# Performance work log

Measured on AMD Instinct MI355X. Metric: run time of the kernel, lower is better.

The kernel has to match this reference:

```python
import jax, jax.numpy as jnp
import numpy as np

N, IN_DIM, HIDDEN, CLASSES, HEADS, E = 4096, 256, 512, 256, 4, 131072
HD = IN_DIM // HEADS


def setup_inputs() -> dict:
    key = jax.random.key(0)
    ks = jax.random.split(key, 16)
    s = 0.02
    x = jax.random.normal(ks[0], (N, IN_DIM), dtype=jnp.float32)
    edge_index = jax.random.randint(ks[1], (2, E), 0, N, dtype=jnp.int64)
    return {
        "x": x,
        "edge_index": edge_index,
        # GCNConv 1: in_dim -> hidden
        "gcn1_w": jax.random.normal(ks[2], (IN_DIM, HIDDEN), dtype=jnp.float32) * s,
        "gcn1_b": jnp.zeros((HIDDEN,), dtype=jnp.float32),
        # GCNConv 2: hidden -> hidden
        "gcn2_w": jax.random.normal(ks[3], (HIDDEN, HIDDEN), dtype=jnp.float32) * s,
        "gcn2_b": jnp.zeros((HIDDEN,), dtype=jnp.float32),
        # final Linear hidden -> classes
        "lin_w": jax.random.normal(ks[4], (HIDDEN, CLASSES), dtype=jnp.float32) * s,
        "lin_b": jnp.zeros((CLASSES,), dtype=jnp.float32),
        # MultiheadAttention packed in-projection (q,k,v) and out-projection
        "in_proj_w": jax.random.normal(ks[5], (3 * IN_DIM, IN_DIM), dtype=jnp.float32) * s,
        "in_proj_b": jnp.zeros((3 * IN_DIM,), dtype=jnp.float32),
        "out_proj_w": jax.random.normal(ks[6], (IN_DIM, IN_DIM), dtype=jnp.float32) * s,
        "out_proj_b": jnp.zeros((IN_DIM,), dtype=jnp.float32),
        # project: in_dim -> classes
        "proj_w": jax.random.normal(ks[7], (IN_DIM, CLASSES), dtype=jnp.float32) * s,
        "proj_b": jnp.zeros((CLASSES,), dtype=jnp.float32),
    }


def gcn_conv(x, src, dst, norm, w, b):
    # PyG GCNConv: transform, then normalized scatter-add aggregation
    h = x @ w                                   # [N+?, F] -> use gathered below
    msg = h[src] * norm[:, None]                # [E+N, F]
    out = jax.ops.segment_sum(msg, dst, num_segments=N)
    return out + b


def mha(x, in_proj_w, in_proj_b, out_proj_w, out_proj_b):
    qkv = x @ in_proj_w.T + in_proj_b           # [N, 3*IN_DIM]
    q, k, v = jnp.split(qkv, 3, axis=-1)
    # [N, IN_DIM] -> [HEADS, N, HD]
    q = q.reshape(N, HEADS, HD).transpose(1, 0, 2)
    k = k.reshape(N, HEADS, HD).transpose(1, 0, 2)
    v = v.reshape(N, HEADS, HD).transpose(1, 0, 2)
    scores = jnp.einsum("hqd,hkd->hqk", q, k) / jnp.sqrt(jnp.float32(HD))
    attn = jax.nn.softmax(scores, axis=-1)      # [HEADS, N, N]
    o = jnp.einsum("hqk,hkd->hqd", attn, v)     # [HEADS, N, HD]
    o = o.transpose(1, 0, 2).reshape(N, IN_DIM)
    return o @ out_proj_w.T + out_proj_b


def reference(x, edge_index, gcn1_w, gcn1_b, gcn2_w, gcn2_b, lin_w, lin_b,
              in_proj_w, in_proj_b, out_proj_w, out_proj_b, proj_w, proj_b):
    # --- GCN normalization with self-loops (computed once, shared by both convs) ---
    loop = jnp.arange(N, dtype=edge_index.dtype)
    src = jnp.concatenate([edge_index[0], loop])  # [E+N]
    dst = jnp.concatenate([edge_index[1], loop])
    deg = jax.ops.segment_sum(jnp.ones_like(dst, dtype=jnp.float32), dst, num_segments=N)
    dinv = jnp.where(deg > 0, jax.lax.rsqrt(deg), 0.0)
    norm = dinv[src] * dinv[dst]                  # [E+N]

    # --- GNN branch ---
    h = jax.nn.relu(gcn_conv(x, src, dst, norm, gcn1_w, gcn1_b))
    h = jax.nn.relu(gcn_conv(h, src, dst, norm, gcn2_w, gcn2_b))
    x_gnn = h @ lin_w + lin_b                     # [N, CLASSES]

    # --- Transformer branch ---
    x_tf = mha(x, in_proj_w, in_proj_b, out_proj_w, out_proj_b)
    x_proj = x_tf @ proj_w + proj_b               # [N, CLASSES]

    return jax.nn.relu(x_gnn + x_proj)
```

## Files before the change

### kernel.cpp

```cpp
#include <hip/hip_runtime.h>
#include <hip/hip_bf16.h>

#define N_NODES 4096
#define IN_DIM  256
#define HIDDEN  512
#define CLASSES 256
#define HEADS   4
#define HD      64
#define NEDGE   131072
#define NMASK   (N_NODES - 1)

typedef __attribute__((ext_vector_type(8))) short bf16x8_t;
typedef __attribute__((ext_vector_type(4))) float f32x4_t;

__device__ inline ushort f2bf(float f) {
    union { float f; uint u; } v; v.f = f;
    uint r = v.u + 0x7FFF + ((v.u >> 16) & 1);
    return (ushort)(r >> 16);
}
__device__ inline float bf2f(ushort u) {
    union { uint u; float f; } v; v.u = (uint)u << 16; return v.f;
}

__global__ void zero_i_k(int* __restrict__ p, int n) {
    int i = blockIdx.x * 256 + threadIdx.x;
    if (i < n) p[i] = 0;
}
__global__ void hist_k(const int* __restrict__ dst, int* __restrict__ cnt) {
    int i = blockIdx.x * 256 + threadIdx.x;
    if (i < NEDGE) atomicAdd(&cnt[dst[i] & NMASK], 1);
}
__global__ __launch_bounds__(256) void scan_k(const int* __restrict__ cnt,
                                              int* __restrict__ rowptr,
                                              float* __restrict__ dinv) {
    __shared__ int part[256];
    const int t = threadIdx.x;
    const int base = t * 16;
    int local[16];
    int s = 0;
    #pragma unroll
    for (int u = 0; u < 16; ++u) { local[u] = cnt[base + u]; s += local[u]; }
    part[t] = s;
    __syncthreads();
    if (t == 0) {
        int acc = 0;
        for (int i = 0; i < 256; ++i) { int v = part[i]; part[i] = acc; acc += v; }
    }
    __syncthreads();
    int acc = part[t];
    #pragma unroll
    for (int u = 0; u < 16; ++u) {
        rowptr[base + u] = acc;
        acc += local[u];
        dinv[base + u] = rsqrtf((float)local[u] + 1.0f);
    }
    if (t == 255) rowptr[N_NODES] = acc;
}
__global__ void scatter_k(const int* __restrict__ src, const int* __restrict__ dst,
                          const int* __restrict__ rowptr, int* __restrict__ tail,
                          int* __restrict__ ssrc) {
    int e = blockIdx.x * 256 + threadIdx.x;
    if (e >= NEDGE) return;
    int d = dst[e] & NMASK;
    int pos = rowptr[d] + atomicAdd(&tail[d], 1);
    ssrc[pos] = src[e] & NMASK;
}

__global__ void split_k(const float* __restrict__ in, ushort* __restrict__ hi,
                        ushort* __restrict__ lo, int n4) {
    int i = blockIdx.x * 256 + threadIdx.x;
    if (i >= n4) return;
    float4 v = ((const float4*)in)[i];
    ushort4 h, l;
    h.x = f2bf(v.x); l.x = f2bf(v.x - bf2f(h.x));
    h.y = f2bf(v.y); l.y = f2bf(v.y - bf2f(h.y));
    h.z = f2bf(v.z); l.z = f2bf(v.z - bf2f(h.z));
    h.w = f2bf(v.w); l.w = f2bf(v.w - bf2f(h.w));
    ((ushort4*)hi)[i] = h;
    ((ushort4*)lo)[i] = l;
}

__global__ __launch_bounds__(256) void tsplit_k(const float* __restrict__ W,
                                                ushort* __restrict__ th,
                                                ushort* __restrict__ tl,
                                                int K, int N) {
    __shared__ float T[64][68];
    const int k0 = blockIdx.x * 64, n0 = blockIdx.y * 64;
    const int t = threadIdx.x;
    {
        const int r = t >> 2, q = (t & 3) * 16;
        const float* src = W + (size_t)(k0 + r) * N + n0 + q;
        #pragma unroll
        for (int i = 0; i < 4; ++i)
            *(float4*)&T[r][q + i * 4] = *(const float4*)(src + i * 4);
    }
    __syncthreads();
    const int n = t >> 2, kq = (t & 3) * 16;
    ushort hh[16], ll[16];
    #pragma unroll
    for (int i = 0; i < 16; ++i) {
        float v = T[kq + i][n];
        ushort h = f2bf(v);
        hh[i] = h; ll[i] = f2bf(v - bf2f(h));
    }
    ushort* ph = th + (size_t)(n0 + n) * K + k0 + kq;
    ushort* pl = tl + (size_t)(n0 + n) * K + k0 + kq;
    #pragma unroll
    for (int i = 0; i < 16; ++i) { ph[i] = hh[i]; pl[i] = ll[i]; }
}

template<int MODE>
__global__ __launch_bounds__(256) void gemm_sp_k(
    const ushort* __restrict__ Ah, const ushort* __restrict__ Al,
    const ushort* __restrict__ Bh, const ushort* __restrict__ Bl,
    const float* __restrict__ bias, const float* src,
    void* o1, void* o2, void* o3, int M, int N, int K)
{
    __shared__ ushort AsH[64][32], AsL[64][32], BsH[64][32], BsL[64][32];
    const int tid = threadIdx.x;
    const int w = tid >> 6, lane = tid & 63, g = lane >> 4, c = lane & 15;
    const int wr = w >> 1, wc = w & 1;
    const int m0 = blockIdx.x * 64, n0 = blockIdx.y * 64;
    const int sr = tid >> 2, sq = (tid & 3) * 8;

    f32x4_t acc[2][2];
    #pragma unroll
    for (int i = 0; i < 2; ++i)
        #pragma unroll
        for (int j = 0; j < 2; ++j) { acc[i][j][0]=0.f; acc[i][j][1]=0.f; acc[i][j][2]=0.f; acc[i][j][3]=0.f; }

    for (int k0 = 0; k0 < K; k0 += 32) {
        __syncthreads();
        *(bf16x8_t*)&AsH[sr][sq] = *(const bf16x8_t*)(Ah + (size_t)(m0 + sr) * K + k0 + sq);
        *(bf16x8_t*)&AsL[sr][sq] = *(const bf16x8_t*)(Al + (size_t)(m0 + sr) * K + k0 + sq);
        *(bf16x8_t*)&BsH[sr][sq] = *(const bf16x8_t*)(Bh + (size_t)(n0 + sr) * K + k0 + sq);
        *(bf16x8_t*)&BsL[sr][sq] = *(const bf16x8_t*)(Bl + (size_t)(n0 + sr) * K + k0 + sq);
        __syncthreads();

        bf16x8_t aH[2], aL[2], bH[2], bL[2];
        #pragma unroll
        for (int mr = 0; mr < 2; ++mr) {
            aH[mr] = *(const bf16x8_t*)&AsH[wr * 32 + mr * 16 + c][g * 8];
            aL[mr] = *(const bf16x8_t*)&AsL[wr * 32 + mr * 16 + c][g * 8];
        }
        #pragma unroll
        for (int nr = 0; nr < 2; ++nr) {
            bH[nr] = *(const bf16x8_t*)&BsH[wc * 32 + nr * 16 + c][g * 8];
            bL[nr] = *(const bf16x8_t*)&BsL[wc * 32 + nr * 16 + c][g * 8];
        }
        #pragma unroll
        for (int mr = 0; mr < 2; ++mr)
            #pragma unroll
            for (int nr = 0; nr < 2; ++nr) {
                acc[mr][nr] = __builtin_amdgcn_mfma_f32_16x16x32_bf16(aH[mr], bH[nr], acc[mr][nr], 0, 0, 0);
                acc[mr][nr] = __builtin_amdgcn_mfma_f32_16x16x32_bf16(aH[mr], bL[nr], acc[mr][nr], 0, 0, 0);
                acc[mr][nr] = __builtin_amdgcn_mfma_f32_16x16x32_bf16(aL[mr], bH[nr], acc[mr][nr], 0, 0, 0);
            }
    }

    #pragma unroll
    for (int mr = 0; mr < 2; ++mr)
        #pragma unroll
        for (int nr = 0; nr < 2; ++nr) {
            const int col = n0 + wc * 32 + nr * 16 + c;
            #pragma unroll
            for (int j = 0; j < 4; ++j) {
                const int row = m0 + wr * 32 + mr * 16 + g * 4 + j;
                float v = acc[mr][nr][j];
                if (MODE != 3) v += bias[col];
                if (MODE == 0) {
                    ((float*)o1)[(size_t)row * N + col] = v;
                } else if (MODE == 1) {
                    v += src[(size_t)row * N + col];
                    ((float*)o1)[(size_t)row * N + col] = fmaxf(v, 0.f);
                } else if (MODE == 2 || MODE == 3) {
                    ushort h = f2bf(v);
                    ((ushort*)o1)[(size_t)row * N + col] = h;
                    ((ushort*)o2)[(size_t)row * N + col] = f2bf(v - bf2f(h));
                } else {
                    if (col < 256) {
                        ((ushort*)o1)[(size_t)row * 256 + col] = f2bf(v * 0.125f);
                    } else if (col < 512) {
                        const int d  = col - 256;
                        const int hh = d >> 6, dl = d & 63;
                        const int ks = dl >> 5, gg = (dl >> 3) & 3, jj = dl & 7;
                        const size_t idx = ((size_t)(hh * 256 + (row >> 4)) * 2 + ks) * 512
                                         + (gg * 16 + (row & 15)) * 8 + jj;
                        ((ushort*)o2)[idx] = f2bf(v);
                    } else {
                        const int d  = col - 512;
                        const int hh = d >> 6, cl = d & 63;
                        const int d0 = cl >> 4, cc = cl & 15;
                        const int rl = row & 63;
                        const int ks = rl >> 5, gg = (rl >> 3) & 3, jj = rl & 7;
                        const size_t idx = (size_t)(hh * 64 + (row >> 6)) * 4096
                                         + d0 * 1024 + ks * 512 + (gg * 16 + cc) * 8 + jj;
                        ((ushort*)o3)[idx] = f2bf(v);
                    }
                }
            }
        }
}

#define PF_K(KB, KTIDX)                                                        \
    {                                                                          \
        const ushort* kb_ = kcol + (size_t)(KTIDX) * 4096;                     \
        KB[0][0] = *(const bf16x8_t*)(kb_);                                    \
        KB[0][1] = *(const bf16x8_t*)(kb_ + 512);                              \
        KB[1][0] = *(const bf16x8_t*)(kb_ + 1024);                             \
        KB[1][1] = *(const bf16x8_t*)(kb_ + 1536);                             \
        KB[2][0] = *(const bf16x8_t*)(kb_ + 2048);                             \
        KB[2][1] = *(const bf16x8_t*)(kb_ + 2560);                             \
        KB[3][0] = *(const bf16x8_t*)(kb_ + 3072);                             \
        KB[3][1] = *(const bf16x8_t*)(kb_ + 3584);                             \
    }

#define ATTN_TILE(KB, KT)                                                      \
    {                                                                          \
        const ushort* vb_ = vcol + (size_t)(KT) * 4096;                        \
        bf16x8_t vf[4][2];                                                     \
        _Pragma("unroll")                                                      \
        for (int d0 = 0; d0 < 4; ++d0) {                                       \
            vf[d0][0] = *(const bf16x8_t*)(vb_ + d0 * 1024);                   \
            vf[d0][1] = *(const bf16x8_t*)(vb_ + d0 * 1024 + 512);             \
        }                                                                      \
        f32x4_t s[4];                                                          \
        _Pragma("unroll")                                                      \
        for (int t = 0; t < 4; ++t) {                                          \
            f32x4_t a; a[0] = 0.f; a[1] = 0.f; a[2] = 0.f; a[3] = 0.f;         \
            a = __builtin_amdgcn_mfma_f32_16x16x32_bf16(qf0, KB[t][0], a, 0, 0, 0); \
            a = __builtin_amdgcn_mfma_f32_16x16x32_bf16(qf1, KB[t][1], a, 0, 0, 0); \
            s[t] = a;                                                          \
        }                                                                      \
        _Pragma("unroll")                                                      \
        for (int r = 0; r < 4; ++r) {                                          \
            float p0 = __expf(s[0][r]);                                        \
            float p1 = __expf(s[1][r]);                                        \
            float p2 = __expf(s[2][r]);                                        \
            float p3 = __expf(s[3][r]);                                        \
            float sum = p0 + p1 + p2 + p3;                                     \
            sum += __shfl_xor(sum, 1);                                         \
            sum += __shfl_xor(sum, 2);                                         \
            sum += __shfl_xor(sum, 4);                                         \
            sum += __shfl_xor(sum, 8);                                         \
            l[r] += sum;                                                       \
            ushort* pr = &Ps[g * 4 + r][c];                                    \
            pr[0]  = f2bf(p0);                                                 \
            pr[16] = f2bf(p1);                                                 \
            pr[32] = f2bf(p2);                                                 \
            pr[48] = f2bf(p3);                                                 \
        }                                                                      \
        bf16x8_t pa0 = *(const bf16x8_t*)&Ps[c][g * 8];                        \
        bf16x8_t pa1 = *(const bf16x8_t*)&Ps[c][g * 8 + 32];                   \
        _Pragma("unroll")                                                      \
        for (int d0 = 0; d0 < 4; ++d0) {                                       \
            o[d0] = __builtin_amdgcn_mfma_f32_16x16x32_bf16(pa0, vf[d0][0], o[d0], 0, 0, 0); \
            o[d0] = __builtin_amdgcn_mfma_f32_16x16x32_bf16(pa1, vf[d0][1], o[d0], 0, 0, 0); \
        }                                                                      \
    }

__global__ __launch_bounds__(64, 3) void attn5_k(const ushort* __restrict__ qb,
                                                 const ushort* __restrict__ kfrag,
                                                 const ushort* __restrict__ vfrag,
                                                 float* __restrict__ po0,
                                                 float* __restrict__ po1,
                                                 float* __restrict__ po2,
                                                 float* __restrict__ pl)
{
    __shared__ ushort Ps[16][72];

    const int q0   = blockIdx.x * 16;
    const int h    = blockIdx.y;
    const int sp   = blockIdx.z;
    const int kt_beg = sp * 22;
    const int kt_end = min(64, kt_beg + 22);
    const int lane = threadIdx.x;
    const int g    = lane >> 4;
    const int c    = lane & 15;

    const ushort* qp = qb + (size_t)(q0 + c) * 256 + h * 64 + g * 8;
    const bf16x8_t qf0 = *(const bf16x8_t*)(qp);
    const bf16x8_t qf1 = *(const bf16x8_t*)(qp + 32);

    f32x4_t o[4];
    float l[4];
    #pragma unroll
    for (int r = 0; r < 4; ++r) {
        l[r] = 0.f;
        o[r][0] = 0.f; o[r][1] = 0.f; o[r][2] = 0.f; o[r][3] = 0.f;
    }

    const ushort* kcol = kfrag + (size_t)h * 262144 + lane * 8;
    const ushort* vcol = vfrag + (size_t)h * 262144 + lane * 8;

    bf16x8_t kbA[4][2], kbB[4][2];
    PF_K(kbA, kt_beg)

    for (int kt = kt_beg; kt < kt_end; kt += 2) {
        PF_K(kbB, kt + 1)
        ATTN_TILE(kbA, kt)
        {
            const int ktn2 = min(kt + 2, kt_end - 1);
            PF_K(kbA, ktn2)
        }
        ATTN_TILE(kbB, kt + 1)
    }

    float* po = (sp == 0) ? po0 : (sp == 1) ? po1 : po2;
    #pragma unroll
    for (int r = 0; r < 4; ++r) {
        float* op = po + ((size_t)h * 4096 + q0 + g * 4 + r) * 64 + c;
        #pragma unroll
        for (int d0 = 0; d0 < 4; ++d0)
            op[16 * d0] = o[d0][r];
    }
    if (c == 0) {
        #pragma unroll
        for (int r = 0; r < 4; ++r)
            pl[(size_t)(sp * 4 + h) * 4096 + q0 + g * 4 + r] = l[r];
    }
}

__global__ __launch_bounds__(256) void comb3_k(const float* __restrict__ po0,
                                               const float* __restrict__ po1,
                                               const float* __restrict__ po2,
                                               const float* __restrict__ pl,
                                               ushort* __restrict__ aoh,
                                               ushort* __restrict__ aol)
{
    int idx = blockIdx.x * 256 + threadIdx.x;
    int row = idx >> 4;
    int h = row >> 12, q = row & 4095;
    int dq = (idx & 15) * 4;
    float l0 = pl[(size_t)(0 * 4 + h) * 4096 + q];
    float l1 = pl[(size_t)(1 * 4 + h) * 4096 + q];
    float l2 = pl[(size_t)(2 * 4 + h) * 4096 + q];
    float inv = 1.0f / (l0 + l1 + l2);
    float4 o0 = *(const float4*)(po0 + (size_t)row * 64 + dq);
    float4 o1 = *(const float4*)(po1 + (size_t)row * 64 + dq);
    float4 o2 = *(const float4*)(po2 + (size_t)row * 64 + dq);
    float vx = (o0.x + o1.x + o2.x) * inv;
    float vy = (o0.y + o1.y + o2.y) * inv;
    float vz = (o0.z + o1.z + o2.z) * inv;
    float vw = (o0.w + o1.w + o2.w) * inv;
    size_t oi = (size_t)q * 256 + h * 64 + dq;
    ushort4 H, L;
    H.x = f2bf(vx); L.x = f2bf(vx - bf2f(H.x));
    H.y = f2bf(vy); L.y = f2bf(vy - bf2f(H.y));
    H.z = f2bf(vz); L.z = f2bf(vz - bf2f(H.z));
    H.w = f2bf(vw); L.w = f2bf(vw - bf2f(H.w));
    *(ushort4*)(aoh + oi) = H;
    *(ushort4*)(aol + oi) = L;
}

__global__ __launch_bounds__(128) void csr_agg2_k(const ushort* __restrict__ hh,
                                                  const ushort* __restrict__ hl,
                                                  const int* __restrict__ rowptr,
                                                  const int* __restrict__ ssrc,
                                                  const float* __restrict__ dinv,
                                                  const float* __restrict__ bias,
                                                  ushort* __restrict__ oh,
                                                  ushort* __restrict__ ol) {
    __shared__ int   nbr[64];
    __shared__ float wnb[64];
    const int d = blockIdx.x;
    const int c = threadIdx.x;
    const int beg = rowptr[d], end = rowptr[d + 1];

    float4 acc = {0.f, 0.f, 0.f, 0.f};
    for (int j0 = beg; j0 < end; j0 += 64) {
        const int mcnt = min(64, end - j0);
        if (c < mcnt) {
            int s = ssrc[j0 + c];
            nbr[c] = s;
            wnb[c] = dinv[s];
        }
        __syncthreads();
        for (int u = 0; u < mcnt; ++u) {
            const int s = nbr[u];
            const float w = wnb[u];
            ushort4 vh = *(const ushort4*)(hh + (size_t)s * 512 + c * 4);
            ushort4 vl = *(const ushort4*)(hl + (size_t)s * 512 + c * 4);
            acc.x += w * (bf2f(vh.x) + bf2f(vl.x));
            acc.y += w * (bf2f(vh.y) + bf2f(vl.y));
            acc.z += w * (bf2f(vh.z) + bf2f(vl.z));
            acc.w += w * (bf2f(vh.w) + bf2f(vl.w));
        }
        __syncthreads();
    }

    const float wd = dinv[d];
    const float wd2 = wd * wd;
    ushort4 sh = *(const ushort4*)(hh + (size_t)d * 512 + c * 4);
    ushort4 sl = *(const ushort4*)(hl + (size_t)d * 512 + c * 4);
    float4 bv = *((const float4*)bias + c);
    float r0 = fmaxf(acc.x * wd + wd2 * (bf2f(sh.x) + bf2f(sl.x)) + bv.x, 0.f);
    float r1 = fmaxf(acc.y * wd + wd2 * (bf2f(sh.y) + bf2f(sl.y)) + bv.y, 0.f);
    float r2 = fmaxf(acc.z * wd + wd2 * (bf2f(sh.z) + bf2f(sl.z)) + bv.z, 0.f);
    float r3 = fmaxf(acc.w * wd + wd2 * (bf2f(sh.w) + bf2f(sl.w)) + bv.w, 0.f);
    ushort4 H, L;
    H.x = f2bf(r0); L.x = f2bf(r0 - bf2f(H.x));
    H.y = f2bf(r1); L.y = f2bf(r1 - bf2f(H.y));
    H.z = f2bf(r2); L.z = f2bf(r2 - bf2f(H.z));
    H.w = f2bf(r3); L.w = f2bf(r3 - bf2f(H.w));
    *(ushort4*)(oh + (size_t)d * 512 + c * 4) = H;
    *(ushort4*)(ol + (size_t)d * 512 + c * 4) = L;
}

extern "C" void kernel_launch(void* const* d_in, const int* in_sizes, int n_in,
                              void* d_out, int out_size, void* d_ws, size_t ws_size,
                              hipStream_t stream)
{
    const float* x          = (const float*)d_in[0];
    const int*   eidx       = (const int*)d_in[1];
    const float* gcn1_w     = (const float*)d_in[2];
    const float* gcn1_b     = (const float*)d_in[3];
    const float* gcn2_w     = (const float*)d_in[4];
    const float* gcn2_b     = (const float*)d_in[5];
    const float* lin_w      = (const float*)d_in[6];
    const float* lin_b      = (const float*)d_in[7];
    const float* in_proj_w  = (const float*)d_in[8];
    const float* in_proj_b  = (const float*)d_in[9];
    const float* out_proj_w = (const float*)d_in[10];
    const float* out_proj_b = (const float*)d_in[11];
    const float* proj_w     = (const float*)d_in[12];
    const float* proj_b     = (const float*)d_in[13];
    float* out = (float*)d_out;

    const int* esrc = eidx;
    const int* edst = eidx + NEDGE;

    char* base = (char*)d_ws;
    size_t off = 0;
    auto take = [&](size_t bytes) -> char* {
        char* p = base + off;
        off = (off + bytes + 255) & ~(size_t)255;
        return p;
    };

    int*   cnt    = (int*)take(N_NODES * 4);
    int*   tail   = (int*)take(N_NODES * 4);
    int*   rowptr = (int*)take((N_NODES + 8) * 4);
    int*   ssrc   = (int*)take(NEDGE * 4);
    float* dinv   = (float*)take(N_NODES * 4);
    float* pl     = (float*)take(3 * HEADS * N_NODES * 4);

    ushort* wreg = (ushort*)take(2 * 1024 * 1024);
    ushort* ipW_h = wreg;
    ushort* ipW_l = ipW_h + 768 * 256;
    ushort* opW_h = ipW_l + 768 * 256;
    ushort* opW_l = opW_h + 256 * 256;
    ushort* pjT_h = opW_l + 256 * 256;
    ushort* pjT_l = pjT_h + 256 * 256;
    ushort* g1T_h = wreg;
    ushort* g1T_l = g1T_h + 512 * 256;
    ushort* g2T_h = g1T_l + 512 * 256;
    ushort* g2T_l = g2T_h + 512 * 512;
    ushort* lT_h  = g2T_l + 512 * 512;
    ushort* lT_l  = lT_h + 256 * 512;

    ushort* xs_h = (ushort*)take(N_NODES * IN_DIM * 2);
    ushort* xs_l = (ushort*)take(N_NODES * IN_DIM * 2);

    char* R2 = take(8 * 1024 * 1024);
    ushort* qb    = (ushort*)R2;
    ushort* kfrag = qb + (size_t)N_NODES * 256;
    ushort* vfrag = kfrag + (size_t)1024 * 1024;
    ushort* ao_h  = (ushort*)R2;
    ushort* ao_l  = ao_h + (size_t)N_NODES * IN_DIM;
    ushort* Ph    = (ushort*)R2;
    ushort* Pl    = Ph + (size_t)N_NODES * HIDDEN;

    char* R3 = take(8 * 1024 * 1024);
    float* po1 = (float*)R3;
    float* po2 = (float*)(R3 + 4 * 1024 * 1024);
    ushort* xt_h = (ushort*)R3;
    ushort* xt_l = xt_h + (size_t)N_NODES * IN_DIM;
    ushort* Qh   = (ushort*)R3;
    ushort* Ql   = Qh + (size_t)N_NODES * HIDDEN;

    float* po0 = out;

    zero_i_k<<<(2 * N_NODES + 255) / 256, 256, 0, stream>>>(cnt, 2 * N_NODES);
    hist_k<<<(NEDGE + 255) / 256, 256, 0, stream>>>(edst, cnt);
    scan_k<<<1, 256, 0, stream>>>(cnt, rowptr, dinv);
    scatter_k<<<(NEDGE + 255) / 256, 256, 0, stream>>>(esrc, edst, rowptr, tail, ssrc);

    split_k<<<(N_NODES * IN_DIM / 4 + 255) / 256, 256, 0, stream>>>(x, xs_h, xs_l, N_NODES * IN_DIM / 4);
    split_k<<<(768 * 256 / 4 + 255) / 256, 256, 0, stream>>>(in_proj_w, ipW_h, ipW_l, 768 * 256 / 4);
    split_k<<<(256 * 256 / 4 + 255) / 256, 256, 0, stream>>>(out_proj_w, opW_h, opW_l, 256 * 256 / 4);
    tsplit_k<<<dim3(4, 4), 256, 0, stream>>>(proj_w, pjT_h, pjT_l, 256, 256);

    gemm_sp_k<4><<<dim3(64, 12), 256, 0, stream>>>(xs_h, xs_l, ipW_h, ipW_l,
        in_proj_b, nullptr, qb, kfrag, vfrag, N_NODES, 768, 256);
    attn5_k<<<dim3(256, 4, 3), 64, 0, stream>>>(qb, kfrag, vfrag, po0, po1, po2, pl);
    comb3_k<<<(HEADS * N_NODES * 16) / 256, 256, 0, stream>>>(po0, po1, po2, pl, ao_h, ao_l);
    gemm_sp_k<2><<<dim3(64, 4), 256, 0, stream>>>(ao_h, ao_l, opW_h, opW_l,
        out_proj_b, nullptr, xt_h, xt_l, nullptr, N_NODES, 256, 256);
    gemm_sp_k<0><<<dim3(64, 4), 256, 0, stream>>>(xt_h, xt_l, pjT_h, pjT_l,
        proj_b, nullptr, out, nullptr, nullptr, N_NODES, 256, 256);

    tsplit_k<<<dim3(4, 8), 256, 0, stream>>>(gcn1_w, g1T_h, g1T_l, 256, 512);
    tsplit_k<<<dim3(8, 8), 256, 0, stream>>>(gcn2_w, g2T_h, g2T_l, 512, 512);
    tsplit_k<<<dim3(8, 4), 256, 0, stream>>>(lin_w, lT_h, lT_l, 512, 256);

    gemm_sp_k<3><<<dim3(64, 8), 256, 0, stream>>>(xs_h, xs_l, g1T_h, g1T_l,
        nullptr, nullptr, Ph, Pl, nullptr, N_NODES, HIDDEN, IN_DIM);
    csr_agg2_k<<<N_NODES, 128, 0, stream>>>(Ph, Pl, rowptr, ssrc, dinv, gcn1_b, Qh, Ql);
    gemm_sp_k<3><<<dim3(64, 8), 256, 0, stream>>>(Qh, Ql, g2T_h, g2T_l,
        nullptr, nullptr, Ph, Pl, nullptr, N_NODES, HIDDEN, HIDDEN);
    csr_agg2_k<<<N_NODES, 128, 0, stream>>>(Ph, Pl, rowptr, ssrc, dinv, gcn2_b, Qh, Ql);

    gemm_sp_k<1><<<dim3(64, 4), 256, 0, stream>>>(Qh, Ql, lT_h, lT_l,
        lin_b, out, out, nullptr, nullptr, N_NODES, CLASSES, HIDDEN);
}
```

Baseline: 304.0 us.

## Fold out/proj weights into one matrix and process 32 queries per attention block

Precomputes the product of proj_w and out_proj_w (plus a combined bias) so the attention output needs one 4096x256x256 GEMM instead of two, removing an intermediate write and read. The attention kernel now handles two 16-row query tiles per wave, reusing each loaded K/V fragment twice and halving the grid. The cost is a few small setup kernels, a different rounding path through the folded weight, and higher register pressure (occupancy hint lowered from 3 to 2).

```diff
diff --git a/kernel.cpp b/kernel.cpp
--- a/kernel.cpp
+++ b/kernel.cpp
@@ -107,6 +107,17 @@
     ushort* pl = tl + (size_t)(n0 + n) * K + k0 + kq;
     #pragma unroll
     for (int i = 0; i < 16; ++i) { ph[i] = hh[i]; pl[i] = ll[i]; }
+}
+
+__global__ __launch_bounds__(256) void bcomb_k(const float* __restrict__ opb,
+                                               const float* __restrict__ pjw,
+                                               const float* __restrict__ pjb,
+                                               float* __restrict__ bp) {
+    const int c = threadIdx.x;
+    float s = pjb[c];
+    for (int i = 0; i < 256; ++i)
+        s += opb[i] * pjw[(size_t)i * 256 + c];
+    bp[c] = s;
 }
 
 template<int MODE>
@@ -224,42 +235,65 @@
             vf[d0][0] = *(const bf16x8_t*)(vb_ + d0 * 1024);                   \
             vf[d0][1] = *(const bf16x8_t*)(vb_ + d0 * 1024 + 512);             \
         }                                                                      \
-        f32x4_t s[4];                                                          \
+        f32x4_t sA[4], sB[4];                                                  \
         _Pragma("unroll")                                                      \
         for (int t = 0; t < 4; ++t) {                                          \
             f32x4_t a; a[0] = 0.f; a[1] = 0.f; a[2] = 0.f; a[3] = 0.f;         \
-            a = __builtin_amdgcn_mfma_f32_16x16x32_bf16(qf0, KB[t][0], a, 0, 0, 0); \
-            a = __builtin_amdgcn_mfma_f32_16x16x32_bf16(qf1, KB[t][1], a, 0, 0, 0); \
-            s[t] = a;                                                          \
+            a = __builtin_amdgcn_mfma_f32_16x16x32_bf16(qfA0, KB[t][0], a, 0, 0, 0); \
+            a = __builtin_amdgcn_mfma_f32_16x16x32_bf16(qfA1, KB[t][1], a, 0, 0, 0); \
+            sA[t] = a;                                                         \
+            f32x4_t b; b[0] = 0.f; b[1] = 0.f; b[2] = 0.f; b[3] = 0.f;         \
+            b = __builtin_amdgcn_mfma_f32_16x16x32_bf16(qfB0, KB[t][0], b, 0, 0, 0); \
+            b = __builtin_amdgcn_mfma_f32_16x16x32_bf16(qfB1, KB[t][1], b, 0, 0, 0); \
+            sB[t] = b;                                                         \
         }                                                                      \
         _Pragma("unroll")                                                      \
         for (int r = 0; r < 4; ++r) {                                          \
-            float p0 = __expf(s[0][r]);                                        \
-            float p1 = __expf(s[1][r]);                                        \
-            float p2 = __expf(s[2][r]);                                        \
-            float p3 = __expf(s[3][r]);                                        \
+            float p0 = __expf(sA[0][r]);                                       \
+            float p1 = __expf(sA[1][r]);                                       \
+            float p2 = __expf(sA[2][r]);                                       \
+            float p3 = __expf(sA[3][r]);                                       \
             float sum = p0 + p1 + p2 + p3;                                     \
             sum += __shfl_xor(sum, 1);                                         \
             sum += __shfl_xor(sum, 2);                                         \
             sum += __shfl_xor(sum, 4);                                         \
             sum += __shfl_xor(sum, 8);                                         \
-            l[r] += sum;                                                       \
+            lA[r] += sum;                                                      \
             ushort* pr = &Ps[g * 4 + r][c];                                    \
             pr[0]  = f2bf(p0);                                                 \
             pr[16] = f2bf(p1);                                                 \
             pr[32] = f2bf(p2);                                                 \
             pr[48] = f2bf(p3);                                                 \
+            float u0 = __expf(sB[0][r]);                                       \
+            float u1 = __expf(sB[1][r]);                                       \
+            float u2 = __expf(sB[2][r]);                                       \
+            float u3 = __expf(sB[3][r]);                                       \
+            float sm2 = u0 + u1 + u2 + u3;                                     \
+            sm2 += __shfl_xor(sm2, 1);                                         \
+            sm2 += __shfl_xor(sm2, 2);                                         \
+            sm2 += __shfl_xor(sm2, 4);                                         \
+            sm2 += __shfl_xor(sm2, 8);                                         \
+            lB[r] += sm2;                                                      \
+            ushort* pr2 = &Ps[16 + g * 4 + r][c];                              \
+            pr2[0]  = f2bf(u0);                                                \
+            pr2[16] = f2bf(u1);                                                \
+            pr2[32] = f2bf(u2);                                                \
+            pr2[48] = f2bf(u3);                                                \
         }                                                                      \
-        bf16x8_t pa0 = *(const bf16x8_t*)&Ps[c][g * 8];                        \
-        bf16x8_t pa1 = *(const bf16x8_t*)&Ps[c][g * 8 + 32];                   \
+        bf16x8_t paA0 = *(const bf16x8_t*)&Ps[c][g * 8];                       \
+        bf16x8_t paA1 = *(const bf16x8_t*)&Ps[c][g * 8 + 32];                  \
+        bf16x8_t paB0 = *(const bf16x8_t*)&Ps[16 + c][g * 8];                  \
+        bf16x8_t paB1 = *(const bf16x8_t*)&Ps[16 + c][g * 8 + 32];             \
         _Pragma("unroll")                                                      \
         for (int d0 = 0; d0 < 4; ++d0) {                                       \
-            o[d0] = __builtin_amdgcn_mfma_f32_16x16x32_bf16(pa0, vf[d0][0], o[d0], 0, 0, 0); \
-            o[d0] = __builtin_amdgcn_mfma_f32_16x16x32_bf16(pa1, vf[d0][1], o[d0], 0, 0, 0); \
+            oA[d0] = __builtin_amdgcn_mfma_f32_16x16x32_bf16(paA0, vf[d0][0], oA[d0], 0, 0, 0); \
+            oA[d0] = __builtin_amdgcn_mfma_f32_16x16x32_bf16(paA1, vf[d0][1], oA[d0], 0, 0, 0); \
+            oB[d0] = __builtin_amdgcn_mfma_f32_16x16x32_bf16(paB0, vf[d0][0], oB[d0], 0, 0, 0); \
+            oB[d0] = __builtin_amdgcn_mfma_f32_16x16x32_bf16(paB1, vf[d0][1], oB[d0], 0, 0, 0); \
         }                                                                      \
     }
 
-__global__ __launch_bounds__(64, 3) void attn5_k(const ushort* __restrict__ qb,
+__global__ __launch_bounds__(64, 2) void attn6_k(const ushort* __restrict__ qb,
                                                  const ushort* __restrict__ kfrag,
                                                  const ushort* __restrict__ vfrag,
                                                  float* __restrict__ po0,
@@ -267,9 +301,9 @@
                                                  float* __restrict__ po2,
                                                  float* __restrict__ pl)
 {
-    __shared__ ushort Ps[16][72];
-
-    const int q0   = blockIdx.x * 16;
+    __shared__ ushort Ps[32][72];
+
+    const int q0   = blockIdx.x * 32;
     const int h    = blockIdx.y;
     const int sp   = blockIdx.z;
     const int kt_beg = sp * 22;
@@ -278,16 +312,20 @@
     const int g    = lane >> 4;
     const int c    = lane & 15;
 
-    const ushort* qp = qb + (size_t)(q0 + c) * 256 + h * 64 + g * 8;
-    const bf16x8_t qf0 = *(const bf16x8_t*)(qp);
-    const bf16x8_t qf1 = *(const bf16x8_t*)(qp + 32);
-
-    f32x4_t o[4];
-    float l[4];
+    const ushort* qpA = qb + (size_t)(q0 + c) * 256 + h * 64 + g * 8;
+    const ushort* qpB = qb + (size_t)(q0 + 16 + c) * 256 + h * 64 + g * 8;
+    const bf16x8_t qfA0 = *(const bf16x8_t*)(qpA);
+    const bf16x8_t qfA1 = *(const bf16x8_t*)(qpA + 32);
+    const bf16x8_t qfB0 = *(const bf16x8_t*)(qpB);
+    const bf16x8_t qfB1 = *(const bf16x8_t*)(qpB + 32);
+
+    f32x4_t oA[4], oB[4];
+    float lA[4], lB[4];
     #pragma unroll
     for (int r = 0; r < 4; ++r) {
-        l[r] = 0.f;
-        o[r][0] = 0.f; o[r][1] = 0.f; o[r][2] = 0.f; o[r][3] = 0.f;
+        lA[r] = 0.f; lB[r] = 0.f;
+        oA[r][0] = 0.f; oA[r][1] = 0.f; oA[r][2] = 0.f; oA[r][3] = 0.f;
+        oB[r][0] = 0.f; oB[r][1] = 0.f; oB[r][2] = 0.f; oB[r][3] = 0.f;
     }
 
     const ushort* kcol = kfrag + (size_t)h * 262144 + lane * 8;
@@ -309,15 +347,20 @@
     float* po = (sp == 0) ? po0 : (sp == 1) ? po1 : po2;
     #pragma unroll
     for (int r = 0; r < 4; ++r) {
-        float* op = po + ((size_t)h * 4096 + q0 + g * 4 + r) * 64 + c;
-        #pragma unroll
-        for (int d0 = 0; d0 < 4; ++d0)
-            op[16 * d0] = o[d0][r];
+        float* opA = po + ((size_t)h * 4096 + q0 + g * 4 + r) * 64 + c;
+        float* opB = po + ((size_t)h * 4096 + q0 + 16 + g * 4 + r) * 64 + c;
+        #pragma unroll
+        for (int d0 = 0; d0 < 4; ++d0) {
+            opA[16 * d0] = oA[d0][r];
+            opB[16 * d0] = oB[d0][r];
+        }
     }
     if (c == 0) {
         #pragma unroll
-        for (int r = 0; r < 4; ++r)
-            pl[(size_t)(sp * 4 + h) * 4096 + q0 + g * 4 + r] = l[r];
+        for (int r = 0; r < 4; ++r) {
+            pl[(size_t)(sp * 4 + h) * 4096 + q0 + g * 4 + r]      = lA[r];
+            pl[(size_t)(sp * 4 + h) * 4096 + q0 + 16 + g * 4 + r] = lB[r];
+        }
     }
 }
 
@@ -444,14 +487,17 @@
     int*   ssrc   = (int*)take(NEDGE * 4);
     float* dinv   = (float*)take(N_NODES * 4);
     float* pl     = (float*)take(3 * HEADS * N_NODES * 4);
+    float* bp     = (float*)take(CLASSES * 4);
 
     ushort* wreg = (ushort*)take(2 * 1024 * 1024);
     ushort* ipW_h = wreg;
     ushort* ipW_l = ipW_h + 768 * 256;
-    ushort* opW_h = ipW_l + 768 * 256;
-    ushort* opW_l = opW_h + 256 * 256;
-    ushort* pjT_h = opW_l + 256 * 256;
+    ushort* opT_h = ipW_l + 768 * 256;
+    ushort* opT_l = opT_h + 256 * 256;
+    ushort* pjT_h = opT_l + 256 * 256;
     ushort* pjT_l = pjT_h + 256 * 256;
+    ushort* WT_h  = pjT_l + 256 * 256;
+    ushort* WT_l  = WT_h + 256 * 256;
     ushort* g1T_h = wreg;
     ushort* g1T_l = g1T_h + 512 * 256;
     ushort* g2T_h = g1T_l + 512 * 256;
@@ -474,10 +520,8 @@
     char* R3 = take(8 * 1024 * 1024);
     float* po1 = (float*)R3;
     float* po2 = (float*)(R3 + 4 * 1024 * 1024);
-    ushort* xt_h = (ushort*)R3;
-    ushort* xt_l = xt_h + (size_t)N_NODES * IN_DIM;
-    ushort* Qh   = (ushort*)R3;
-    ushort* Ql   = Qh + (size_t)N_NODES * HIDDEN;
+    ushort* Qh = (ushort*)R3;
+    ushort* Ql = Qh + (size_t)N_NODES * HIDDEN;
 
     float* po0 = out;
 
@@ -488,17 +532,18 @@
 
     split_k<<<(N_NODES * IN_DIM / 4 + 255) / 256, 256, 0, stream>>>(x, xs_h, xs_l, N_NODES * IN_DIM / 4);
     split_k<<<(768 * 256 / 4 + 255) / 256, 256, 0, stream>>>(in_proj_w, ipW_h, ipW_l, 768 * 256 / 4);
-    split_k<<<(256 * 256 / 4 + 255) / 256, 256, 0, stream>>>(out_proj_w, opW_h, opW_l, 256 * 256 / 4);
+    tsplit_k<<<dim3(4, 4), 256, 0, stream>>>(out_proj_w, opT_h, opT_l, 256, 256);
     tsplit_k<<<dim3(4, 4), 256, 0, stream>>>(proj_w, pjT_h, pjT_l, 256, 256);
+    gemm_sp_k<3><<<dim3(4, 4), 256, 0, stream>>>(pjT_h, pjT_l, opT_h, opT_l,
+        nullptr, nullptr, WT_h, WT_l, nullptr, 256, 256, 256);
+    bcomb_k<<<1, 256, 0, stream>>>(out_proj_b, proj_w, proj_b, bp);
 
     gemm_sp_k<4><<<dim3(64, 12), 256, 0, stream>>>(xs_h, xs_l, ipW_h, ipW_l,
         in_proj_b, nullptr, qb, kfrag, vfrag, N_NODES, 768, 256);
-    attn5_k<<<dim3(256, 4, 3), 64, 0, stream>>>(qb, kfrag, vfrag, po0, po1, po2, pl);
+    attn6_k<<<dim3(128, 4, 3), 64, 0, stream>>>(qb, kfrag, vfrag, po0, po1, po2, pl);
     comb3_k<<<(HEADS * N_NODES * 16) / 256, 256, 0, stream>>>(po0, po1, po2, pl, ao_h, ao_l);
-    gemm_sp_k<2><<<dim3(64, 4), 256, 0, stream>>>(ao_h, ao_l, opW_h, opW_l,
-        out_proj_b, nullptr, xt_h, xt_l, nullptr, N_NODES, 256, 256);
-    gemm_sp_k<0><<<dim3(64, 4), 256, 0, stream>>>(xt_h, xt_l, pjT_h, pjT_l,
-        proj_b, nullptr, out, nullptr, nullptr, N_NODES, 256, 256);
+    gemm_sp_k<0><<<dim3(64, 4), 256, 0, stream>>>(ao_h, ao_l, WT_h, WT_l,
+        bp, nullptr, out, nullptr, nullptr, N_NODES, 256, 256);
 
     tsplit_k<<<dim3(4, 8), 256, 0, stream>>>(gcn1_w, g1T_h, g1T_l, 256, 512);
     tsplit_k<<<dim3(8, 8), 256, 0, stream>>>(gcn2_w, g2T_h, g2T_l, 512, 512);
```

Result: slower. 326.8 us (+7.5%).
